# Kernel optimization log

Hardware: AMD Instinct MI355X
Metric: run time of the kernel (lower is better)

The kernel has to match this reference:

```python
import jax, jax.numpy as jnp
import numpy as np

N_NODES = 100000


def _gcn_conv(h, src, dst, W, b, n_nodes):
    """PyG GCNConv with add_self_loops=True, symmetric normalization.
    out = D^-1/2 (A + I) D^-1/2 (h W) + b, aggregating src->dst."""
    h = h @ W  # transform first (out_dim <= in_dim), as PyG does
    ones = jnp.ones(src.shape[0], dtype=h.dtype)
    deg = jax.ops.segment_sum(ones, dst, num_segments=n_nodes) + 1.0  # +1 self loop
    dinv = jax.lax.rsqrt(deg)
    coef = dinv[src] * dinv[dst]  # per-edge norm
    agg = jax.ops.segment_sum(h[src] * coef[:, None], dst, num_segments=n_nodes)
    agg = agg + h * (dinv * dinv)[:, None]  # self-loop term: dinv_i^2 * h_i
    return agg + b


def setup_inputs() -> dict:
    key = jax.random.key(0)
    k1, k2, k3, k4 = jax.random.split(key, 4)
    x = jax.random.normal(k1, (N_NODES, 256), dtype=jnp.float32)
    edge_index = jax.random.randint(k2, (2, 1600000), 0, N_NODES, dtype=jnp.int64)
    W1 = jax.random.normal(k3, (256, 128), dtype=jnp.float32) * (1.0 / np.sqrt(256))
    b1 = jnp.zeros((128,), dtype=jnp.float32)
    W2 = jax.random.normal(k4, (128, 64), dtype=jnp.float32) * (1.0 / np.sqrt(128))
    b2 = jnp.zeros((64,), dtype=jnp.float32)
    return {"x": x, "edge_index": edge_index, "W1": W1, "b1": b1, "W2": W2, "b2": b2}


def reference(x, edge_index, W1, b1, W2, b2):
    src, dst = edge_index[0], edge_index[1]
    h = jax.nn.relu(_gcn_conv(x, src, dst, W1, b1, N_NODES))
    # dropout is identity in eval mode
    h = _gcn_conv(h, src, dst, W2, b2, N_NODES)
    return jax.nn.log_softmax(h, axis=1)
```

## Files before the change

kernel.cpp:

```cpp
#include <hip/hip_runtime.h>
#include <hip/hip_bf16.h>


#define N_NODES 100000
#define F_IN 256
#define F_MID 128
#define F_OUT 64

#define BSHIFT 8
#define BNODES 256
#define NBUCKETS ((N_NODES + BNODES - 1) / BNODES)
#define BCAP 6144
#define EPB 4096

typedef __attribute__((ext_vector_type(8))) short short8;
typedef __attribute__((ext_vector_type(4))) float f32x4;

__device__ inline ushort bf16_rne(float f) {
    uint u = __float_as_uint(f);
    u += 0x7FFF + ((u >> 16) & 1);
    return (ushort)(u >> 16);
}
__device__ inline float lo16(uint r) { return __uint_as_float(r << 16); }
__device__ inline float hi16(uint r) { return __uint_as_float(r & 0xffff0000u); }
__device__ inline uint pack_bf2(float a, float b) {
    return (uint)bf16_rne(a) | ((uint)bf16_rne(b) << 16);
}


__global__ __launch_bounds__(256)
void bucket_scatter_kernel(const int* __restrict__ src, const int* __restrict__ dst,
                           int* __restrict__ bcur, uint* __restrict__ ebuf, int E) {
    __shared__ int hist[512], ps[512], cur[512];
    __shared__ int base[NBUCKETS];
    __shared__ uint   eLoc[EPB];
    __shared__ ushort bLoc[EPB];
    int t = threadIdx.x;
    int e0 = blockIdx.x * EPB;
    int e1 = e0 + EPB; if (e1 > E) e1 = E;
    int ne = e1 - e0;

    for (int i = t; i < 512; i += 256) hist[i] = 0;
    __syncthreads();
    for (int i = t; i < ne; i += 256) atomicAdd(&hist[dst[e0 + i] >> BSHIFT], 1);
    __syncthreads();
    ps[t] = hist[t]; ps[t + 256] = hist[t + 256];
    __syncthreads();
#pragma unroll
    for (int off = 1; off < 512; off <<= 1) {
        int i0 = t, i1 = t + 256;
        int v0 = (i0 >= off) ? ps[i0 - off] : 0;
        int v1 = (i1 >= off) ? ps[i1 - off] : 0;
        __syncthreads();
        ps[i0] += v0; ps[i1] += v1;
        __syncthreads();
    }
    {
        int ex0 = ps[t] - hist[t];
        int ex1 = ps[t + 256] - hist[t + 256];
        __syncthreads();
        ps[t] = ex0; ps[t + 256] = ex1;
        cur[t] = ex0; cur[t + 256] = ex1;
    }
    __syncthreads();
    for (int i = t; i < ne; i += 256) {
        int d = dst[e0 + i], s = src[e0 + i];
        int b = d >> BSHIFT;
        int p = atomicAdd(&cur[b], 1);
        eLoc[p] = ((uint)(d & (BNODES - 1)) << 17) | (uint)s;
        bLoc[p] = (ushort)b;
    }
    __syncthreads();
    for (int b = t; b < NBUCKETS; b += 256) {
        int h = hist[b];
        base[b] = h ? atomicAdd(&bcur[b], h) : 0;
    }
    __syncthreads();
    for (int i = t; i < ne; i += 256) {
        int b = bLoc[i];
        int d = base[b] + (i - ps[b]);
        if (d < BCAP) ebuf[(size_t)b * BCAP + d] = eLoc[i];
    }
}

__global__ __launch_bounds__(256)
void bucket_sort_kernel(const uint* __restrict__ ebuf, const int* __restrict__ bcur,
                        int* __restrict__ ssrc, int* __restrict__ rs, int* __restrict__ cnt,
                        float* __restrict__ dinv, int n) {
    __shared__ uint eL[BCAP];
    __shared__ int  sLoc[BCAP];
    __shared__ int hist[BNODES], ps[BNODES];
    int b = blockIdx.x, t = threadIdx.x;
    int nb = bcur[b];
    if (nb > BCAP) nb = BCAP;
    for (int i = t; i < nb; i += 256) eL[i] = ebuf[(size_t)b * BCAP + i];
    hist[t] = 0;
    __syncthreads();
    for (int i = t; i < nb; i += 256) atomicAdd(&hist[eL[i] >> 17], 1);
    __syncthreads();
    ps[t] = hist[t];
    __syncthreads();
#pragma unroll
    for (int off = 1; off < BNODES; off <<= 1) {
        int v = (t >= off) ? ps[t - off] : 0;
        __syncthreads();
        ps[t] += v;
        __syncthreads();
    }
    int excl = ps[t] - hist[t];
    int node = b * BNODES + t;
    if (node < n) {
        rs[node] = b * BCAP + excl;
        cnt[node] = hist[t];
        dinv[node] = 1.0f / sqrtf((float)hist[t] + 1.0f);
    }
    __syncthreads();
    ps[t] = excl;
    __syncthreads();
    for (int i = t; i < nb; i += 256) {
        uint e = eL[i];
        int d = e >> 17;
        int p = atomicAdd(&ps[d], 1);
        sLoc[p] = (int)(e & 0x1FFFF);
    }
    __syncthreads();
    for (int i = t; i < nb; i += 256) ssrc[(size_t)b * BCAP + i] = sLoc[i];
}

__global__ __launch_bounds__(256)
void wprep_kernel(const float* __restrict__ W1, const float* __restrict__ W2,
                  short8* __restrict__ W1f, short8* __restrict__ W2f) {
    int b = blockIdx.x;
    if (b < 16) {
        int f = b * 256 + threadIdx.x;
        int k0 = f >> 9, nt = (f >> 6) & 7, ln = f & 63;
        int kbase = k0 * 32 + (ln >> 4) * 8;
        int n = nt * 16 + (ln & 15);
        short8 fr;
#pragma unroll
        for (int j = 0; j < 8; ++j) fr[j] = (short)bf16_rne(W1[(kbase + j) * F_MID + n]);
        W1f[f] = fr;
    } else {
        int f = (b - 16) * 256 + threadIdx.x;
        int k0 = f >> 8, nt = (f >> 6) & 3, ln = f & 63;
        int kbase = k0 * 32 + (ln >> 4) * 8;
        int n = nt * 16 + (ln & 15);
        short8 fr;
#pragma unroll
        for (int j = 0; j < 8; ++j) fr[j] = (short)bf16_rne(W2[(kbase + j) * F_OUT + n]);
        W2f[f] = fr;
    }
}


__global__ __launch_bounds__(512, 4)
void gemm1_kernel(const float* __restrict__ A, const short8* __restrict__ Wf,
                  const float* __restrict__ dinv, ushort* __restrict__ C,
                  int M) {
    __shared__ ushort Abuf[2][128 * 64];
    int tid = threadIdx.x;
    int lane = tid & 63, w = tid >> 6;
    int m0 = blockIdx.x * 128;

    int o0 = tid * 2;
    int srow = o0 >> 3;
    int gr = m0 + srow; if (gr >= M) gr = m0;
    int cl0 = o0 & 7, cl1 = cl0 + 1;
    int cg0 = cl0 ^ (srow & 7), cg1 = cl1 ^ (srow & 7);
    const float* arow = &A[(size_t)gr * F_IN];

    float4 rv[2][2];
    rv[0][0] = ((const float4*)(arow + cg0 * 8))[0];
    rv[0][1] = ((const float4*)(arow + cg0 * 8))[1];
    rv[1][0] = ((const float4*)(arow + cg1 * 8))[0];
    rv[1][1] = ((const float4*)(arow + cg1 * 8))[1];

    {
        short8 pk;
        pk[0] = (short)bf16_rne(rv[0][0].x); pk[1] = (short)bf16_rne(rv[0][0].y);
        pk[2] = (short)bf16_rne(rv[0][0].z); pk[3] = (short)bf16_rne(rv[0][0].w);
        pk[4] = (short)bf16_rne(rv[0][1].x); pk[5] = (short)bf16_rne(rv[0][1].y);
        pk[6] = (short)bf16_rne(rv[0][1].z); pk[7] = (short)bf16_rne(rv[0][1].w);
        *(short8*)&Abuf[0][o0 * 8] = pk;
        pk[0] = (short)bf16_rne(rv[1][0].x); pk[1] = (short)bf16_rne(rv[1][0].y);
        pk[2] = (short)bf16_rne(rv[1][0].z); pk[3] = (short)bf16_rne(rv[1][0].w);
        pk[4] = (short)bf16_rne(rv[1][1].x); pk[5] = (short)bf16_rne(rv[1][1].y);
        pk[6] = (short)bf16_rne(rv[1][1].z); pk[7] = (short)bf16_rne(rv[1][1].w);
        *(short8*)&Abuf[0][(o0 + 1) * 8] = pk;
    }
    __syncthreads();

    f32x4 acc[8];
#pragma unroll
    for (int nt = 0; nt < 8; ++nt) acc[nt] = (f32x4){0.f, 0.f, 0.f, 0.f};

    int arow16 = w * 16 + (lane & 15);
    int asw = arow16 & 7;
    int abase = arow16 * 8;

#pragma unroll
    for (int kc = 0; kc < 4; ++kc) {
        int b = kc & 1;
        if (kc < 3) {
            const float* s0 = arow + (kc + 1) * 64 + cg0 * 8;
            const float* s1 = arow + (kc + 1) * 64 + cg1 * 8;
            rv[0][0] = ((const float4*)s0)[0];
            rv[0][1] = ((const float4*)s0)[1];
            rv[1][0] = ((const float4*)s1)[0];
            rv[1][1] = ((const float4*)s1)[1];
            asm volatile("" ::: "memory");
        }
#pragma unroll
        for (int kk = 0; kk < 2; ++kk) {
            int k0 = kc * 2 + kk;
            int c = kk * 4 + (lane >> 4);
            short8 af = *(const short8*)&Abuf[b][(abase + (c ^ asw)) * 8];
#pragma unroll
            for (int nt = 0; nt < 8; ++nt) {
                short8 bfr = Wf[(k0 * 8 + nt) * 64 + lane];
                acc[nt] = __builtin_amdgcn_mfma_f32_16x16x32_bf16(af, bfr, acc[nt], 0, 0, 0);
            }
        }
        if (kc < 3) {
            short8 pk;
            pk[0] = (short)bf16_rne(rv[0][0].x); pk[1] = (short)bf16_rne(rv[0][0].y);
            pk[2] = (short)bf16_rne(rv[0][0].z); pk[3] = (short)bf16_rne(rv[0][0].w);
            pk[4] = (short)bf16_rne(rv[0][1].x); pk[5] = (short)bf16_rne(rv[0][1].y);
            pk[6] = (short)bf16_rne(rv[0][1].z); pk[7] = (short)bf16_rne(rv[0][1].w);
            *(short8*)&Abuf[b ^ 1][o0 * 8] = pk;
            pk[0] = (short)bf16_rne(rv[1][0].x); pk[1] = (short)bf16_rne(rv[1][0].y);
            pk[2] = (short)bf16_rne(rv[1][0].z); pk[3] = (short)bf16_rne(rv[1][0].w);
            pk[4] = (short)bf16_rne(rv[1][1].x); pk[5] = (short)bf16_rne(rv[1][1].y);
            pk[6] = (short)bf16_rne(rv[1][1].z); pk[7] = (short)bf16_rne(rv[1][1].w);
            *(short8*)&Abuf[b ^ 1][(o0 + 1) * 8] = pk;
        }
        __syncthreads();
    }

#pragma unroll
    for (int i = 0; i < 4; ++i) {
        int r = blockIdx.x * 128 + w * 16 + (lane >> 4) * 4 + i;
        if (r < M) {
            float dv = dinv[r];
#pragma unroll
            for (int nt = 0; nt < 8; ++nt)
                C[(size_t)r * F_MID + nt * 16 + (lane & 15)] = bf16_rne(dv * acc[nt][i]);
        }
    }
}

__global__ __launch_bounds__(256)
void agg1f_kernel(const uint4* __restrict__ h, const int* __restrict__ rs,
                  const int* __restrict__ cnt, const int* __restrict__ ssrc,
                  const float* __restrict__ dinv, const float* __restrict__ bias,
                  const short8* __restrict__ W2f, ushort* __restrict__ h2, int n) {
    __shared__ __align__(16) ushort rowsL[16][136];
    int w = threadIdx.x >> 6, lane = threadIdx.x & 63;
    int q = lane >> 4, c16 = lane & 15;
    int nbase = blockIdx.x * 16;
    const float4* b4 = (const float4*)bias;
    float4 b0 = b4[c16 * 2], b1v = b4[c16 * 2 + 1];

#pragma unroll
    for (int i = 0; i < 4; ++i) {
        int node = nbase + w * 4 + i;
        bool nOk = (node < n);
        int start = nOk ? rs[node] : 0;
        int c = nOk ? cnt[node] : 0;
        float dn = nOk ? dinv[node] : 0.f;
        float a[8];
#pragma unroll
        for (int k = 0; k < 8; ++k) a[k] = 0.f;

        for (int base = 0; base < c; base += 16) {
            bool p[4];
            int s[4];
            uint4 r[4];
#pragma unroll
            for (int j = 0; j < 4; ++j) {
                int e = base + j * 4 + q;
                p[j] = e < c;
                if (p[j]) s[j] = ssrc[start + e];
            }
#pragma unroll
            for (int j = 0; j < 4; ++j)
                if (p[j]) r[j] = h[(size_t)s[j] * 16 + c16];
#pragma unroll
            for (int j = 0; j < 4; ++j) {
                if (p[j]) {
                    a[0] += lo16(r[j].x); a[1] += hi16(r[j].x);
                    a[2] += lo16(r[j].y); a[3] += hi16(r[j].y);
                    a[4] += lo16(r[j].z); a[5] += hi16(r[j].z);
                    a[6] += lo16(r[j].w); a[7] += hi16(r[j].w);
                }
            }
        }
#pragma unroll
        for (int k = 0; k < 8; ++k) {
            a[k] += __shfl_xor(a[k], 16);
            a[k] += __shfl_xor(a[k], 32);
        }
        if (q == 0) {
            short8 pk;
            if (nOk) {
                uint4 sr = h[(size_t)node * 16 + c16];
                float o0 = fmaxf(fmaf(dn, a[0] + lo16(sr.x), b0.x), 0.f);
                float o1 = fmaxf(fmaf(dn, a[1] + hi16(sr.x), b0.y), 0.f);
                float o2 = fmaxf(fmaf(dn, a[2] + lo16(sr.y), b0.z), 0.f);
                float o3 = fmaxf(fmaf(dn, a[3] + hi16(sr.y), b0.w), 0.f);
                float o4 = fmaxf(fmaf(dn, a[4] + lo16(sr.z), b1v.x), 0.f);
                float o5 = fmaxf(fmaf(dn, a[5] + hi16(sr.z), b1v.y), 0.f);
                float o6 = fmaxf(fmaf(dn, a[6] + lo16(sr.w), b1v.z), 0.f);
                float o7 = fmaxf(fmaf(dn, a[7] + hi16(sr.w), b1v.w), 0.f);
                pk[0] = (short)bf16_rne(o0); pk[1] = (short)bf16_rne(o1);
                pk[2] = (short)bf16_rne(o2); pk[3] = (short)bf16_rne(o3);
                pk[4] = (short)bf16_rne(o4); pk[5] = (short)bf16_rne(o5);
                pk[6] = (short)bf16_rne(o6); pk[7] = (short)bf16_rne(o7);
            } else {
                pk = (short8){0, 0, 0, 0, 0, 0, 0, 0};
            }
            *(short8*)&rowsL[w * 4 + i][c16 * 8] = pk;
        }
    }
    __syncthreads();

    f32x4 acc = (f32x4){0.f, 0.f, 0.f, 0.f};
    int ar = lane & 15;
#pragma unroll
    for (int k0 = 0; k0 < 4; ++k0) {
        short8 af = *(const short8*)&rowsL[ar][k0 * 32 + (lane >> 4) * 8];
        short8 bfr = W2f[(k0 * 4 + w) * 64 + lane];
        acc = __builtin_amdgcn_mfma_f32_16x16x32_bf16(af, bfr, acc, 0, 0, 0);
    }
#pragma unroll
    for (int i = 0; i < 4; ++i) {
        int r = (lane >> 4) * 4 + i;
        int node = nbase + r;
        if (node < n) {
            float dv = dinv[node];
            h2[(size_t)node * F_OUT + w * 16 + (lane & 15)] = bf16_rne(dv * acc[i]);
        }
    }
}

__global__ __launch_bounds__(256)
void agg2_kernel(const uint2* __restrict__ h, const int* __restrict__ rs,
                 const int* __restrict__ cnt, const int* __restrict__ ssrc,
                 const float* __restrict__ dinv, const float* __restrict__ bias,
                 float4* __restrict__ out4, int n) {
    int w = threadIdx.x >> 6, lane = threadIdx.x & 63;
    int q = lane >> 4, c16 = lane & 15;
    int nodeA = blockIdx.x * 8 + w * 2;
    int nodeB = nodeA + 1;
    bool okA = (nodeA < n), okB = (nodeB < n);
    if (!okA) return;
    int startA = rs[nodeA], cA = cnt[nodeA];
    int startB = okB ? rs[nodeB] : 0, cB = okB ? cnt[nodeB] : 0;
    float dnA = dinv[nodeA];
    float dnB = okB ? dinv[nodeB] : 0.f;
    float aA[4], aB[4];
#pragma unroll
    for (int i = 0; i < 4; ++i) { aA[i] = 0.f; aB[i] = 0.f; }

    int cm = cA > cB ? cA : cB;
    for (int base = 0; base < cm; base += 16) {
        bool pA[4], pB[4];
        int sA[4], sB[4];
        uint2 rA[4], rB[4];
#pragma unroll
        for (int j = 0; j < 4; ++j) {
            int e = base + j * 4 + q;
            pA[j] = e < cA;
            pB[j] = e < cB;
            if (pA[j]) sA[j] = ssrc[startA + e];
            if (pB[j]) sB[j] = ssrc[startB + e];
        }
#pragma unroll
        for (int j = 0; j < 4; ++j) {
            if (pA[j]) rA[j] = h[(size_t)sA[j] * 16 + c16];
            if (pB[j]) rB[j] = h[(size_t)sB[j] * 16 + c16];
        }
#pragma unroll
        for (int j = 0; j < 4; ++j) {
            if (pA[j]) {
                aA[0] += lo16(rA[j].x); aA[1] += hi16(rA[j].x);
                aA[2] += lo16(rA[j].y); aA[3] += hi16(rA[j].y);
            }
            if (pB[j]) {
                aB[0] += lo16(rB[j].x); aB[1] += hi16(rB[j].x);
                aB[2] += lo16(rB[j].y); aB[3] += hi16(rB[j].y);
            }
        }
    }
#pragma unroll
    for (int i = 0; i < 4; ++i) {
        aA[i] += __shfl_xor(aA[i], 16);
        aA[i] += __shfl_xor(aA[i], 32);
        aB[i] += __shfl_xor(aB[i], 16);
        aB[i] += __shfl_xor(aB[i], 32);
    }
    float4 bv = ((const float4*)bias)[c16];
    {
        uint2 sr = h[(size_t)nodeA * 16 + c16];
        float v0 = fmaf(dnA, aA[0] + lo16(sr.x), bv.x);
        float v1 = fmaf(dnA, aA[1] + hi16(sr.x), bv.y);
        float v2 = fmaf(dnA, aA[2] + lo16(sr.y), bv.z);
        float v3 = fmaf(dnA, aA[3] + hi16(sr.y), bv.w);
        float m = fmaxf(fmaxf(v0, v1), fmaxf(v2, v3));
#pragma unroll
        for (int off = 1; off < 16; off <<= 1) m = fmaxf(m, __shfl_xor(m, off));
        float ssum = expf(v0 - m) + expf(v1 - m) + expf(v2 - m) + expf(v3 - m);
#pragma unroll
        for (int off = 1; off < 16; off <<= 1) ssum += __shfl_xor(ssum, off);
        float lg = m + logf(ssum);
        if (q == 0) out4[(size_t)nodeA * 16 + c16] = make_float4(v0 - lg, v1 - lg, v2 - lg, v3 - lg);
    }
    if (okB) {
        uint2 sr = h[(size_t)nodeB * 16 + c16];
        float v0 = fmaf(dnB, aB[0] + lo16(sr.x), bv.x);
        float v1 = fmaf(dnB, aB[1] + hi16(sr.x), bv.y);
        float v2 = fmaf(dnB, aB[2] + lo16(sr.y), bv.z);
        float v3 = fmaf(dnB, aB[3] + hi16(sr.y), bv.w);
        float m = fmaxf(fmaxf(v0, v1), fmaxf(v2, v3));
#pragma unroll
        for (int off = 1; off < 16; off <<= 1) m = fmaxf(m, __shfl_xor(m, off));
        float ssum = expf(v0 - m) + expf(v1 - m) + expf(v2 - m) + expf(v3 - m);
#pragma unroll
        for (int off = 1; off < 16; off <<= 1) ssum += __shfl_xor(ssum, off);
        float lg = m + logf(ssum);
        if (q == 0) out4[(size_t)nodeB * 16 + c16] = make_float4(v0 - lg, v1 - lg, v2 - lg, v3 - lg);
    }
}


extern "C" void kernel_launch(void* const* d_in, const int* in_sizes, int n_in,
                              void* d_out, int out_size, void* d_ws, size_t ws_size,
                              hipStream_t stream) {
    const float* x  = (const float*)d_in[0];
    const int*   ei = (const int*)d_in[1];
    const float* W1 = (const float*)d_in[2];
    const float* b1 = (const float*)d_in[3];
    const float* W2 = (const float*)d_in[4];
    const float* b2 = (const float*)d_in[5];
    float* out = (float*)d_out;

    const int N = N_NODES;
    const int E = in_sizes[1] / 2;
    const int* src = ei;
    const int* dst = ei + E;

    char* ws = (char*)d_ws;
    size_t off = 0;
    auto alloc = [&](size_t bytes) {
        char* p = ws + off;
        off = (off + bytes + 255) & ~(size_t)255;
        return p;
    };
    int*    bcur   = (int*)alloc(NBUCKETS * 4);
    int*    rs     = (int*)alloc(N * 4);
    int*    cnt    = (int*)alloc(N * 4);
    float*  dinv   = (float*)alloc(N * 4);
    short8* W1f    = (short8*)alloc(4096 * 16);
    short8* W2f    = (short8*)alloc(1024 * 16);
    uint*   ebuf   = (uint*)alloc((size_t)NBUCKETS * BCAP * 4);
    int*    ssrc   = (int*)alloc((size_t)NBUCKETS * BCAP * 4);
    uint*   h1     = (uint*)alloc((size_t)N * 64 * 4);
    ushort* h2     = (ushort*)alloc((size_t)N * 64 * 2);

    const int nScatBlocks = (E + EPB - 1) / EPB;
    const int nAgg1Blocks = (N + 15) / 16;
    const int nAgg2Blocks = (N + 7) / 8;
    const int nTiles      = (N + 127) / 128;

    hipMemsetAsync(bcur, 0, NBUCKETS * 4, stream);
    wprep_kernel<<<20, 256, 0, stream>>>(W1, W2, W1f, W2f);

    bucket_scatter_kernel<<<nScatBlocks, 256, 0, stream>>>(src, dst, bcur, ebuf, E);
    bucket_sort_kernel<<<NBUCKETS, 256, 0, stream>>>(ebuf, bcur, ssrc, rs, cnt, dinv, N);

    gemm1_kernel<<<nTiles, 512, 0, stream>>>(x, W1f, dinv, (ushort*)h1, N);
    agg1f_kernel<<<nAgg1Blocks, 256, 0, stream>>>((const uint4*)h1, rs, cnt, ssrc, dinv, b1,
                                                  W2f, h2, N);
    agg2_kernel<<<nAgg2Blocks, 256, 0, stream>>>((const uint2*)h2, rs, cnt, ssrc, dinv, b2,
                                                 (float4*)out, N);
}
```

Baseline: 352.9 us.

## Merge edge bucket scatter and first GEMM into one launch, move dinv scaling into aggregation

Combines the edge bucketing scatter and the first feature GEMM into a single kernel whose blocks are split by index, so the two independent phases can run concurrently. To drop the GEMM's dependency on the degree normalization, the GEMM output is no longer scaled by dinv. Instead the aggregation kernel loads dinv[src] per edge and uses FMAs, and applies dinv to the self-loop term. This adds an extra gather per edge in agg1 and rounds the unscaled product to bf16, which slightly changes numerics.

```diff
diff --git a/kernel.cpp b/kernel.cpp
--- a/kernel.cpp
+++ b/kernel.cpp
@@ -25,62 +25,6 @@
 __device__ inline float hi16(uint r) { return __uint_as_float(r & 0xffff0000u); }
 __device__ inline uint pack_bf2(float a, float b) {
     return (uint)bf16_rne(a) | ((uint)bf16_rne(b) << 16);
-}
-
-
-__global__ __launch_bounds__(256)
-void bucket_scatter_kernel(const int* __restrict__ src, const int* __restrict__ dst,
-                           int* __restrict__ bcur, uint* __restrict__ ebuf, int E) {
-    __shared__ int hist[512], ps[512], cur[512];
-    __shared__ int base[NBUCKETS];
-    __shared__ uint   eLoc[EPB];
-    __shared__ ushort bLoc[EPB];
-    int t = threadIdx.x;
-    int e0 = blockIdx.x * EPB;
-    int e1 = e0 + EPB; if (e1 > E) e1 = E;
-    int ne = e1 - e0;
-
-    for (int i = t; i < 512; i += 256) hist[i] = 0;
-    __syncthreads();
-    for (int i = t; i < ne; i += 256) atomicAdd(&hist[dst[e0 + i] >> BSHIFT], 1);
-    __syncthreads();
-    ps[t] = hist[t]; ps[t + 256] = hist[t + 256];
-    __syncthreads();
-#pragma unroll
-    for (int off = 1; off < 512; off <<= 1) {
-        int i0 = t, i1 = t + 256;
-        int v0 = (i0 >= off) ? ps[i0 - off] : 0;
-        int v1 = (i1 >= off) ? ps[i1 - off] : 0;
-        __syncthreads();
-        ps[i0] += v0; ps[i1] += v1;
-        __syncthreads();
-    }
-    {
-        int ex0 = ps[t] - hist[t];
-        int ex1 = ps[t + 256] - hist[t + 256];
-        __syncthreads();
-        ps[t] = ex0; ps[t + 256] = ex1;
-        cur[t] = ex0; cur[t + 256] = ex1;
-    }
-    __syncthreads();
-    for (int i = t; i < ne; i += 256) {
-        int d = dst[e0 + i], s = src[e0 + i];
-        int b = d >> BSHIFT;
-        int p = atomicAdd(&cur[b], 1);
-        eLoc[p] = ((uint)(d & (BNODES - 1)) << 17) | (uint)s;
-        bLoc[p] = (ushort)b;
-    }
-    __syncthreads();
-    for (int b = t; b < NBUCKETS; b += 256) {
-        int h = hist[b];
-        base[b] = h ? atomicAdd(&bcur[b], h) : 0;
-    }
-    __syncthreads();
-    for (int i = t; i < ne; i += 256) {
-        int b = bLoc[i];
-        int d = base[b] + (i - ps[b]);
-        if (d < BCAP) ebuf[(size_t)b * BCAP + d] = eLoc[i];
-    }
 }
 
 __global__ __launch_bounds__(256)
@@ -152,17 +96,69 @@
     }
 }
 
-
 __global__ __launch_bounds__(512, 4)
-void gemm1_kernel(const float* __restrict__ A, const short8* __restrict__ Wf,
-                  const float* __restrict__ dinv, ushort* __restrict__ C,
-                  int M) {
-    __shared__ ushort Abuf[2][128 * 64];
-    int tid = threadIdx.x;
-    int lane = tid & 63, w = tid >> 6;
-    int m0 = blockIdx.x * 128;
-
-    int o0 = tid * 2;
+void sg_kernel(const int* __restrict__ src, const int* __restrict__ dst,
+               int* __restrict__ bcur, uint* __restrict__ ebuf, int E,
+               const float* __restrict__ A, const short8* __restrict__ Wf,
+               ushort* __restrict__ C, int M, int nScat) {
+    __shared__ __align__(16) char smemRaw[32768];
+    int t = threadIdx.x;
+
+    if ((int)blockIdx.x < nScat) {
+        int* hist = (int*)smemRaw;
+        int* ps   = hist + 512;
+        int* cur  = ps + 512;
+        int* base = cur + 512;
+        uint*   eLoc = (uint*)(base + NBUCKETS);
+        ushort* bLoc = (ushort*)(eLoc + EPB);
+
+        int e0 = blockIdx.x * EPB;
+        int e1 = e0 + EPB; if (e1 > E) e1 = E;
+        int ne = e1 - e0;
+
+        hist[t] = 0;
+        __syncthreads();
+        for (int i = t; i < ne; i += 512) atomicAdd(&hist[dst[e0 + i] >> BSHIFT], 1);
+        __syncthreads();
+        ps[t] = hist[t];
+        __syncthreads();
+#pragma unroll
+        for (int off = 1; off < 512; off <<= 1) {
+            int v = (t >= off) ? ps[t - off] : 0;
+            __syncthreads();
+            ps[t] += v;
+            __syncthreads();
+        }
+        int ex = ps[t] - hist[t];
+        ps[t] = ex; cur[t] = ex;
+        __syncthreads();
+        for (int i = t; i < ne; i += 512) {
+            int d = dst[e0 + i], s = src[e0 + i];
+            int b = d >> BSHIFT;
+            int p = atomicAdd(&cur[b], 1);
+            eLoc[p] = ((uint)(d & (BNODES - 1)) << 17) | (uint)s;
+            bLoc[p] = (ushort)b;
+        }
+        __syncthreads();
+        for (int b = t; b < NBUCKETS; b += 512) {
+            int h = hist[b];
+            base[b] = h ? atomicAdd(&bcur[b], h) : 0;
+        }
+        __syncthreads();
+        for (int i = t; i < ne; i += 512) {
+            int b = bLoc[i];
+            int d = base[b] + (i - ps[b]);
+            if (d < BCAP) ebuf[(size_t)b * BCAP + d] = eLoc[i];
+        }
+        return;
+    }
+
+    ushort* Ab = (ushort*)smemRaw;
+    int lane = t & 63, w = t >> 6;
+    int bx = blockIdx.x - nScat;
+    int m0 = bx * 128;
+
+    int o0 = t * 2;
     int srow = o0 >> 3;
     int gr = m0 + srow; if (gr >= M) gr = m0;
     int cl0 = o0 & 7, cl1 = cl0 + 1;
@@ -181,12 +177,12 @@
         pk[2] = (short)bf16_rne(rv[0][0].z); pk[3] = (short)bf16_rne(rv[0][0].w);
         pk[4] = (short)bf16_rne(rv[0][1].x); pk[5] = (short)bf16_rne(rv[0][1].y);
         pk[6] = (short)bf16_rne(rv[0][1].z); pk[7] = (short)bf16_rne(rv[0][1].w);
-        *(short8*)&Abuf[0][o0 * 8] = pk;
+        *(short8*)&Ab[o0 * 8] = pk;
         pk[0] = (short)bf16_rne(rv[1][0].x); pk[1] = (short)bf16_rne(rv[1][0].y);
         pk[2] = (short)bf16_rne(rv[1][0].z); pk[3] = (short)bf16_rne(rv[1][0].w);
         pk[4] = (short)bf16_rne(rv[1][1].x); pk[5] = (short)bf16_rne(rv[1][1].y);
         pk[6] = (short)bf16_rne(rv[1][1].z); pk[7] = (short)bf16_rne(rv[1][1].w);
-        *(short8*)&Abuf[0][(o0 + 1) * 8] = pk;
+        *(short8*)&Ab[(o0 + 1) * 8] = pk;
     }
     __syncthreads();
 
@@ -214,7 +210,7 @@
         for (int kk = 0; kk < 2; ++kk) {
             int k0 = kc * 2 + kk;
             int c = kk * 4 + (lane >> 4);
-            short8 af = *(const short8*)&Abuf[b][(abase + (c ^ asw)) * 8];
+            short8 af = *(const short8*)&Ab[b * 8192 + (abase + (c ^ asw)) * 8];
 #pragma unroll
             for (int nt = 0; nt < 8; ++nt) {
                 short8 bfr = Wf[(k0 * 8 + nt) * 64 + lane];
@@ -227,24 +223,23 @@
             pk[2] = (short)bf16_rne(rv[0][0].z); pk[3] = (short)bf16_rne(rv[0][0].w);
             pk[4] = (short)bf16_rne(rv[0][1].x); pk[5] = (short)bf16_rne(rv[0][1].y);
             pk[6] = (short)bf16_rne(rv[0][1].z); pk[7] = (short)bf16_rne(rv[0][1].w);
-            *(short8*)&Abuf[b ^ 1][o0 * 8] = pk;
+            *(short8*)&Ab[(b ^ 1) * 8192 + o0 * 8] = pk;
             pk[0] = (short)bf16_rne(rv[1][0].x); pk[1] = (short)bf16_rne(rv[1][0].y);
             pk[2] = (short)bf16_rne(rv[1][0].z); pk[3] = (short)bf16_rne(rv[1][0].w);
             pk[4] = (short)bf16_rne(rv[1][1].x); pk[5] = (short)bf16_rne(rv[1][1].y);
             pk[6] = (short)bf16_rne(rv[1][1].z); pk[7] = (short)bf16_rne(rv[1][1].w);
-            *(short8*)&Abuf[b ^ 1][(o0 + 1) * 8] = pk;
+            *(short8*)&Ab[(b ^ 1) * 8192 + (o0 + 1) * 8] = pk;
         }
         __syncthreads();
     }
 
 #pragma unroll
     for (int i = 0; i < 4; ++i) {
-        int r = blockIdx.x * 128 + w * 16 + (lane >> 4) * 4 + i;
+        int r = m0 + w * 16 + (lane >> 4) * 4 + i;
         if (r < M) {
-            float dv = dinv[r];
 #pragma unroll
             for (int nt = 0; nt < 8; ++nt)
-                C[(size_t)r * F_MID + nt * 16 + (lane & 15)] = bf16_rne(dv * acc[nt][i]);
+                C[(size_t)r * F_MID + nt * 16 + (lane & 15)] = bf16_rne(acc[nt][i]);
         }
     }
 }
@@ -275,6 +270,7 @@
         for (int base = 0; base < c; base += 16) {
             bool p[4];
             int s[4];
+            float ds[4];
             uint4 r[4];
 #pragma unroll
             for (int j = 0; j < 4; ++j) {
@@ -283,15 +279,19 @@
                 if (p[j]) s[j] = ssrc[start + e];
             }
 #pragma unroll
-            for (int j = 0; j < 4; ++j)
-                if (p[j]) r[j] = h[(size_t)s[j] * 16 + c16];
-#pragma unroll
             for (int j = 0; j < 4; ++j) {
                 if (p[j]) {
-                    a[0] += lo16(r[j].x); a[1] += hi16(r[j].x);
-                    a[2] += lo16(r[j].y); a[3] += hi16(r[j].y);
-                    a[4] += lo16(r[j].z); a[5] += hi16(r[j].z);
-                    a[6] += lo16(r[j].w); a[7] += hi16(r[j].w);
+                    r[j] = h[(size_t)s[j] * 16 + c16];
+                    ds[j] = dinv[s[j]];
+                }
+            }
+#pragma unroll
+            for (int j = 0; j < 4; ++j) {
+                if (p[j]) {
+                    a[0] = fmaf(ds[j], lo16(r[j].x), a[0]); a[1] = fmaf(ds[j], hi16(r[j].x), a[1]);
+                    a[2] = fmaf(ds[j], lo16(r[j].y), a[2]); a[3] = fmaf(ds[j], hi16(r[j].y), a[3]);
+                    a[4] = fmaf(ds[j], lo16(r[j].z), a[4]); a[5] = fmaf(ds[j], hi16(r[j].z), a[5]);
+                    a[6] = fmaf(ds[j], lo16(r[j].w), a[6]); a[7] = fmaf(ds[j], hi16(r[j].w), a[7]);
                 }
             }
         }
@@ -304,14 +304,14 @@
             short8 pk;
             if (nOk) {
                 uint4 sr = h[(size_t)node * 16 + c16];
-                float o0 = fmaxf(fmaf(dn, a[0] + lo16(sr.x), b0.x), 0.f);
-                float o1 = fmaxf(fmaf(dn, a[1] + hi16(sr.x), b0.y), 0.f);
-                float o2 = fmaxf(fmaf(dn, a[2] + lo16(sr.y), b0.z), 0.f);
-                float o3 = fmaxf(fmaf(dn, a[3] + hi16(sr.y), b0.w), 0.f);
-                float o4 = fmaxf(fmaf(dn, a[4] + lo16(sr.z), b1v.x), 0.f);
-                float o5 = fmaxf(fmaf(dn, a[5] + hi16(sr.z), b1v.y), 0.f);
-                float o6 = fmaxf(fmaf(dn, a[6] + lo16(sr.w), b1v.z), 0.f);
-                float o7 = fmaxf(fmaf(dn, a[7] + hi16(sr.w), b1v.w), 0.f);
+                float o0 = fmaxf(fmaf(dn, fmaf(dn, lo16(sr.x), a[0]), b0.x), 0.f);
+                float o1 = fmaxf(fmaf(dn, fmaf(dn, hi16(sr.x), a[1]), b0.y), 0.f);
+                float o2 = fmaxf(fmaf(dn, fmaf(dn, lo16(sr.y), a[2]), b0.z), 0.f);
+                float o3 = fmaxf(fmaf(dn, fmaf(dn, hi16(sr.y), a[3]), b0.w), 0.f);
+                float o4 = fmaxf(fmaf(dn, fmaf(dn, lo16(sr.z), a[4]), b1v.x), 0.f);
+                float o5 = fmaxf(fmaf(dn, fmaf(dn, hi16(sr.z), a[5]), b1v.y), 0.f);
+                float o6 = fmaxf(fmaf(dn, fmaf(dn, lo16(sr.w), a[6]), b1v.z), 0.f);
+                float o7 = fmaxf(fmaf(dn, fmaf(dn, hi16(sr.w), a[7]), b1v.w), 0.f);
                 pk[0] = (short)bf16_rne(o0); pk[1] = (short)bf16_rne(o1);
                 pk[2] = (short)bf16_rne(o2); pk[3] = (short)bf16_rne(o3);
                 pk[4] = (short)bf16_rne(o4); pk[5] = (short)bf16_rne(o5);
@@ -467,7 +467,7 @@
     uint*   h1     = (uint*)alloc((size_t)N * 64 * 4);
     ushort* h2     = (ushort*)alloc((size_t)N * 64 * 2);
 
-    const int nScatBlocks = (E + EPB - 1) / EPB;
+    const int nScat       = (E + EPB - 1) / EPB;
     const int nAgg1Blocks = (N + 15) / 16;
     const int nAgg2Blocks = (N + 7) / 8;
     const int nTiles      = (N + 127) / 128;
@@ -475,10 +475,10 @@
     hipMemsetAsync(bcur, 0, NBUCKETS * 4, stream);
     wprep_kernel<<<20, 256, 0, stream>>>(W1, W2, W1f, W2f);
 
-    bucket_scatter_kernel<<<nScatBlocks, 256, 0, stream>>>(src, dst, bcur, ebuf, E);
+    sg_kernel<<<nScat + nTiles, 512, 0, stream>>>(src, dst, bcur, ebuf, E,
+                                                  x, W1f, (ushort*)h1, N, nScat);
     bucket_sort_kernel<<<NBUCKETS, 256, 0, stream>>>(ebuf, bcur, ssrc, rs, cnt, dinv, N);
 
-    gemm1_kernel<<<nTiles, 512, 0, stream>>>(x, W1f, dinv, (ushort*)h1, N);
     agg1f_kernel<<<nAgg1Blocks, 256, 0, stream>>>((const uint4*)h1, rs, cnt, ssrc, dinv, b1,
                                                   W2f, h2, N);
     agg2_kernel<<<nAgg2Blocks, 256, 0, stream>>>((const uint2*)h2, rs, cnt, ssrc, dinv, b2,
```

New measurement: 336.2 us. 1.05x faster.
